# Optimization experiments

Hardware: AMD Instinct MI355X
Metric: run time of the kernel (lower is better)

Reference implementation:

```python
import jax, jax.numpy as jnp
import numpy as np

E = 1024   # embedding_dim
H = 16     # num_head
D = 64     # dim_head (E == H*D)
R = 8      # LoRA rank
BATCH = 2
SEQ = 2048
EPS = 1e-6


def setup_inputs() -> dict:
    key = jax.random.key(0)
    ks = jax.random.split(key, 16)
    s = 0.02
    return {
        "y": jax.random.normal(ks[0], (BATCH, SEQ, E), jnp.float32),
        "Wqkv": jax.random.normal(ks[1], (3 * E, E), jnp.float32) * s,
        "bqkv": jax.random.normal(ks[2], (3 * E,), jnp.float32) * s,
        "Wmsa": jax.random.normal(ks[3], (E, E), jnp.float32) * s,
        "Bq": jax.random.normal(ks[4], (E, R), jnp.float32) * s,
        "Aq": jax.random.normal(ks[5], (R, E), jnp.float32) * s,
        "Bk": jax.random.normal(ks[6], (E, R), jnp.float32) * s,
        "Ak": jax.random.normal(ks[7], (R, E), jnp.float32) * s,
        "Bv": jax.random.normal(ks[8], (E, R), jnp.float32) * s,
        "Av": jax.random.normal(ks[9], (R, E), jnp.float32) * s,
        "Bo": jax.random.normal(ks[10], (E, R), jnp.float32) * s,
        "Ao": jax.random.normal(ks[11], (R, E), jnp.float32) * s,
        "gamma": jnp.ones((E,), jnp.float32),
        "beta": jnp.zeros((E,), jnp.float32),
        "i": 0,
    }


def reference(y, Wqkv, bqkv, Wmsa, Bq, Aq, Bk, Ak, Bv, Av, Bo, Ao, gamma, beta, i):
    B, S, En = y.shape
    # fused QKV projection: nn.Linear -> y @ W.T + b
    qkv = (y @ Wqkv.T + bqkv).reshape(B, S, 3, H, D).transpose(2, 0, 3, 1, 4)
    Q, K, V = qkv[0], qkv[1], qkv[2]          # each [B,H,S,D]

    def lora_delta(Bw, Aw):
        # torch: y @ (B.weight @ A.weight), reshaped to heads
        return (y @ (Bw @ Aw)).reshape(B, S, H, D).transpose(0, 2, 1, 3)

    Q = Q + lora_delta(Bq, Aq)
    K = K + lora_delta(Bk, Ak)
    V = V + lora_delta(Bv, Av)

    scale = jnp.asarray(np.sqrt(D), y.dtype)
    scores = jnp.einsum('bhqd,bhkd->bhqk', Q, K) / scale
    attn = jax.nn.softmax(scores, axis=-1)
    o = jnp.einsum('bhqk,bhkd->bhqd', attn, V)          # [B,H,S,D]
    o = o.transpose(0, 2, 1, 3).reshape(B, S, H * D)    # [B,S,E]

    msa = o @ Wmsa.T + o @ (Bo @ Ao)
    res = msa + y

    mu = jnp.mean(res, axis=-1, keepdims=True)
    var = jnp.var(res, axis=-1, keepdims=True)
    return (res - mu) * jax.lax.rsqrt(var + EPS) * gamma + beta
```

## Files before the change

kernel.cpp:

```cpp
#include <hip/hip_runtime.h>
#include <hip/hip_bf16.h>
#include <stdint.h>

typedef __attribute__((ext_vector_type(8))) short short8;
typedef __attribute__((ext_vector_type(4))) float f32x4;

typedef const __attribute__((address_space(1))) void gv_t;
typedef __attribute__((address_space(3))) void lv_t;

#define SCQ 0.18033688011112042f

__device__ __forceinline__ void gl_lds16(const void* g, void* l) {
    __builtin_amdgcn_global_load_lds((gv_t*)g, (lv_t*)l, 16, 0, 0);
}

__device__ __forceinline__ unsigned short f2bf(float f) {
    union { float f; unsigned int u; } v; v.f = f;
    unsigned int r = v.u + 0x7fffu + ((v.u >> 16) & 1u);
    return (unsigned short)(r >> 16);
}

__device__ __forceinline__ float bf2f(unsigned short u) {
    union { unsigned int i; float f; } v; v.i = ((unsigned int)u) << 16; return v.f;
}

__device__ __forceinline__ unsigned int pack2bf(float a, float b) {
    union { __hip_bfloat162 h2; unsigned int u; } cv;
    cv.h2 = __float22bfloat162_rn(make_float2(a, b));
    return cv.u;
}

__device__ __forceinline__ f32x4 zero4() { f32x4 z = {0.f, 0.f, 0.f, 0.f}; return z; }

__global__ void k_prep(const float* __restrict__ y,
                       const float* __restrict__ Wqkv, const float* __restrict__ Wmsa,
                       const float* __restrict__ Bq, const float* __restrict__ Aq,
                       const float* __restrict__ Bk, const float* __restrict__ Ak,
                       const float* __restrict__ Bv, const float* __restrict__ Av,
                       const float* __restrict__ Bo, const float* __restrict__ Ao,
                       unsigned short* __restrict__ wout, unsigned short* __restrict__ yb) {
    const int bid = blockIdx.x;
    if (bid < 16384) {
        int idx = bid * 256 + threadIdx.x;
        int n = idx >> 10, k = idx & 1023;
        int sel = n >> 10, n0 = n & 1023;
        const float* Bp = (sel == 0) ? Bq : (sel == 1) ? Bk : (sel == 2) ? Bv : Bo;
        const float* Ap = (sel == 0) ? Aq : (sel == 1) ? Ak : (sel == 2) ? Av : Ao;
        float acc = (sel < 3) ? Wqkv[idx] : Wmsa[idx - 3145728];
        float4 b0 = *(const float4*)(Bp + k * 8);
        float4 b1 = *(const float4*)(Bp + k * 8 + 4);
        acc += b0.x * Ap[0 * 1024 + n0] + b0.y * Ap[1 * 1024 + n0]
             + b0.z * Ap[2 * 1024 + n0] + b0.w * Ap[3 * 1024 + n0]
             + b1.x * Ap[4 * 1024 + n0] + b1.y * Ap[5 * 1024 + n0]
             + b1.z * Ap[6 * 1024 + n0] + b1.w * Ap[7 * 1024 + n0];
        wout[idx] = f2bf(acc * ((sel == 0) ? SCQ : 1.0f));
    } else {
        int i = ((bid - 16384) * 256 + threadIdx.x) * 4;
        float4 v = *(const float4*)(y + i);
        union { unsigned short u[4]; uint2 w; } o;
        o.u[0] = f2bf(v.x); o.u[1] = f2bf(v.y); o.u[2] = f2bf(v.z); o.u[3] = f2bf(v.w);
        *(uint2*)(yb + i) = o.w;
    }
}

template <int TM, int EPI, int MINW, int XMAP>
__global__ __launch_bounds__(256, MINW) void k_gemm(const unsigned short* __restrict__ Ag,
                                                    const unsigned short* __restrict__ Bg,
                                                    const float* __restrict__ bias,
                                                    const float* __restrict__ yres,
                                                    unsigned short* __restrict__ vtg,
                                                    void* __restrict__ Cout,
                                                    int M, int N, int K, int Kst) {
    constexpr int WAVES_N = 256 / TM;
    constexpr int WN = TM / 2;
    constexpr int NI = WN / 16;
    constexpr int ACALLS = TM / 64;
    constexpr int ASZ = 2 * TM * 32;
    __shared__ unsigned short SH[ASZ + 2 * 128 * 32];
    unsigned short* As0 = SH;
    unsigned short* Bs0 = SH + ASZ;
    const int flat = threadIdx.x;
    int m0, n0, koff = 0, split = 0;
    if constexpr (XMAP == 1) {
        int id = blockIdx.x, xcd = id & 7, j = id >> 3;
        int yy = (xcd & 3) * 8 + j / 12;
        int xx = (xcd >> 2) * 12 + j % 12;
        m0 = yy * TM; n0 = xx * 128;
    } else if constexpr (XMAP == 2) {
        int id = blockIdx.x, xcd = id & 7, j = id >> 3;
        split = xcd >> 2;
        int yy = (xcd & 3) * 8 + (j >> 3);
        int xx = j & 7;
        m0 = yy * TM; n0 = xx * 128; koff = split * 512;
    } else {
        m0 = blockIdx.y * TM; n0 = blockIdx.x * 128;
    }
    const int lane = flat & 63, wave = flat >> 6;
    const int l16 = lane & 15, quad = lane >> 4;
    const int wm = (wave / WAVES_N) * 64, wn = (wave % WAVES_N) * WN;

    f32x4 acc[4][NI];
    #pragma unroll
    for (int mi = 0; mi < 4; ++mi)
        #pragma unroll
        for (int ni = 0; ni < NI; ++ni) acc[mi][ni] = zero4();

    const unsigned short* ap = Ag + (size_t)(m0 + (flat >> 2)) * Kst + koff + (flat & 3) * 8;
    const unsigned short* bp = Bg + (size_t)(n0 + (flat >> 2)) * Kst + koff + (flat & 3) * 8;
    const size_t rstep = (size_t)64 * Kst;

    #pragma unroll
    for (int c = 0; c < ACALLS; ++c) gl_lds16(ap + c * rstep, &As0[c * 2048 + flat * 8]);
    gl_lds16(bp,         &Bs0[flat * 8]);
    gl_lds16(bp + rstep, &Bs0[2048 + flat * 8]);
    ap += 32; bp += 32;
    __syncthreads();

    for (int k0 = 0; k0 < K; k0 += 32) {
        const int cur = (k0 >> 5) & 1;
        if (k0 + 32 < K) {
            const int nxt = cur ^ 1;
            #pragma unroll
            for (int c = 0; c < ACALLS; ++c) gl_lds16(ap + c * rstep, &As0[nxt * TM * 32 + c * 2048 + flat * 8]);
            gl_lds16(bp,         &Bs0[nxt * 4096 + flat * 8]);
            gl_lds16(bp + rstep, &Bs0[nxt * 4096 + 2048 + flat * 8]);
            ap += 32; bp += 32;
        }

        short8 af[4], bfr[NI];
        #pragma unroll
        for (int i = 0; i < 4; ++i) af[i] = *(const short8*)&As0[cur * TM * 32 + (wm + i * 16 + l16) * 32 + quad * 8];
        #pragma unroll
        for (int i = 0; i < NI; ++i) bfr[i] = *(const short8*)&Bs0[cur * 4096 + (wn + i * 16 + l16) * 32 + quad * 8];
        #pragma unroll
        for (int mi = 0; mi < 4; ++mi)
            #pragma unroll
            for (int ni = 0; ni < NI; ++ni)
                acc[mi][ni] = __builtin_amdgcn_mfma_f32_16x16x32_bf16(af[mi], bfr[ni], acc[mi][ni], 0, 0, 0);

        __syncthreads();
    }

    if constexpr (EPI == 0) {
        unsigned short* C = (unsigned short*)Cout;
        if (n0 < 2048) {
            #pragma unroll
            for (int ni = 0; ni < NI; ++ni) {
                int col = n0 + wn + ni * 16 + l16;
                float bv = bias[col] * ((col < 1024) ? SCQ : 1.0f);
                #pragma unroll
                for (int mi = 0; mi < 4; ++mi) {
                    int row = m0 + wm + mi * 16 + quad * 4;
                    #pragma unroll
                    for (int r = 0; r < 4; ++r)
                        C[(size_t)(row + r) * N + col] = f2bf(acc[mi][ni][r] + bv);
                }
            }
        } else {
            if constexpr (TM == 128) {
                #pragma unroll
                for (int ni = 0; ni < NI; ++ni) {
                    int c = wn + ni * 16 + l16;
                    float bv = bias[n0 + c];
                    int sw = (c & 7) << 3;
                    #pragma unroll
                    for (int mi = 0; mi < 4; ++mi) {
                        int row = wm + mi * 16 + quad * 4;
                        uint2 w;
                        w.x = pack2bf(acc[mi][ni][0] + bv, acc[mi][ni][1] + bv);
                        w.y = pack2bf(acc[mi][ni][2] + bv, acc[mi][ni][3] + bv);
                        *(uint2*)&SH[c * 128 + (row ^ sw)] = w;
                    }
                }
                __syncthreads();
                const int bb = m0 >> 11, ss = m0 & 2047;
                #pragma unroll
                for (int p = 0; p < 4; ++p) {
                    int c = p * 32 + (flat >> 3);
                    int col = n0 + c;
                    int hh = (col - 2048) >> 6, dd = col & 63;
                    unsigned short* dst = vtg + (size_t)(hh * 64 + dd) * 2048
                                              + (size_t)bb * 2097152 + ss;
                    int sw = (c & 7) << 3;
                    #pragma unroll
                    for (int hf = 0; hf < 2; ++hf) {
                        int off = hf * 64 + (flat & 7) * 8;
                        uint4 v = *(const uint4*)&SH[c * 128 + (off ^ sw)];
                        *(uint4*)(dst + off) = v;
                    }
                }
            }
        }
    } else if constexpr (EPI == 1) {
        float* C = (float*)Cout;
        #pragma unroll
        for (int ni = 0; ni < NI; ++ni) {
            int col = n0 + wn + ni * 16 + l16;
            #pragma unroll
            for (int mi = 0; mi < 4; ++mi) {
                int row = m0 + wm + mi * 16 + quad * 4;
                #pragma unroll
                for (int r = 0; r < 4; ++r)
                    C[(size_t)(row + r) * N + col] = acc[mi][ni][r] + yres[(size_t)(row + r) * N + col];
            }
        }
    } else {
        unsigned short* C = (unsigned short*)Cout + (size_t)split * 4194304;
        #pragma unroll
        for (int ni = 0; ni < NI; ++ni) {
            int col = n0 + wn + ni * 16 + l16;
            #pragma unroll
            for (int mi = 0; mi < 4; ++mi) {
                int row = m0 + wm + mi * 16 + quad * 4;
                #pragma unroll
                for (int r = 0; r < 4; ++r)
                    C[(size_t)(row + r) * N + col] = f2bf(acc[mi][ni][r]);
            }
        }
    }
}

__global__ __launch_bounds__(256, 2) void k_attn(const unsigned short* __restrict__ qkv,
                                                 const unsigned short* __restrict__ vtg,
                                                 unsigned short* __restrict__ o) {
    __shared__ unsigned short LDS[16384];
    unsigned short* Qs = LDS;
    unsigned short* Ks0 = LDS;
    unsigned short* Vt0 = LDS + 8192;

    const int t = threadIdx.x;
    const int lane = t & 63, wave = t >> 6;
    const int l16 = lane & 15, quad = lane >> 4;
    const int l8 = l16 & 7;
    const int id = blockIdx.x;
    const int xcd = id & 7, loc = id >> 3;
    const int qb = loc & 15;
    const int P = xcd + 8 * (loc >> 4);
    const int h = P & 15, b = P >> 4;
    const int q0 = qb * 128;

    const unsigned short* qbase = qkv + (size_t)(b * 2048) * 3072 + h * 64;
    const unsigned short* kbase = qbase + 1024;
    const unsigned short* vtbase = vtg + (size_t)((b * 16 + h) * 64) * 2048;

    #pragma unroll
    for (int i = 0; i < 4; ++i) {
        int B = i * 256 + t;
        int row = B >> 3, c = (B & 7) ^ (row & 7);
        gl_lds16(qbase + (size_t)(q0 + row) * 3072 + c * 8, &Qs[B * 8]);
    }

    const int B0 = t, B1 = t + 256;
    const int r0 = B0 >> 3, c0 = (B0 & 7) ^ (r0 & 7);
    const int r1 = B1 >> 3, c1 = (B1 & 7) ^ (r1 & 7);
    const unsigned short* kp0 = kbase + (size_t)r0 * 3072 + c0 * 8;
    const unsigned short* kp1 = kbase + (size_t)r1 * 3072 + c1 * 8;
    const unsigned short* vp0 = vtbase + (size_t)r0 * 2048 + c0 * 8;
    const unsigned short* vp1 = vtbase + (size_t)r1 * 2048 + c1 * 8;

    __syncthreads();

    short8 qf[2][2];
    #pragma unroll
    for (int ni = 0; ni < 2; ++ni)
        #pragma unroll
        for (int kk = 0; kk < 2; ++kk)
            qf[ni][kk] = *(const short8*)&Qs[(wave * 32 + ni * 16 + l16) * 64 + ((kk * 4 + quad) ^ l8) * 8];

    __syncthreads();

    gl_lds16(kp0, &Ks0[B0 * 8]);
    gl_lds16(kp1, &Ks0[B1 * 8]);
    gl_lds16(vp0, &Vt0[B0 * 8]);
    gl_lds16(vp1, &Vt0[B1 * 8]);
    kp0 += 64 * 3072; kp1 += 64 * 3072; vp0 += 64; vp1 += 64;

    f32x4 acc_o[2][4];
    #pragma unroll
    for (int mo = 0; mo < 2; ++mo)
        #pragma unroll
        for (int nd = 0; nd < 4; ++nd) acc_o[mo][nd] = zero4();
    f32x4 acc_l[2] = {zero4(), zero4()};
    const f32x4 Z4 = zero4();
    short8 ones;
    #pragma unroll
    for (int i = 0; i < 8; ++i) ones[i] = (short)0x3F80;

    __syncthreads();

    for (int j = 0; j < 32; ++j) {
        const unsigned short* Ks = Ks0 + (j & 1) * 4096;
        const unsigned short* Vt = Vt0 + (j & 1) * 4096;

        if (j < 31) {
            unsigned short* Kn = Ks0 + ((j + 1) & 1) * 4096;
            unsigned short* Vn = Vt0 + ((j + 1) & 1) * 4096;
            gl_lds16(kp0, &Kn[B0 * 8]);
            gl_lds16(kp1, &Kn[B1 * 8]);
            gl_lds16(vp0, &Vn[B0 * 8]);
            gl_lds16(vp1, &Vn[B1 * 8]);
            kp0 += 64 * 3072; kp1 += 64 * 3072; vp0 += 64; vp1 += 64;
        }

        f32x4 sacc[4][2];
        #pragma unroll
        for (int mi = 0; mi < 4; ++mi) {
            short8 kf0 = *(const short8*)&Ks[(mi * 16 + l16) * 64 + ((0 + quad) ^ l8) * 8];
            short8 kf1 = *(const short8*)&Ks[(mi * 16 + l16) * 64 + ((4 + quad) ^ l8) * 8];
            #pragma unroll
            for (int ni = 0; ni < 2; ++ni) {
                sacc[mi][ni] = __builtin_amdgcn_mfma_f32_16x16x32_bf16(kf0, qf[ni][0], Z4, 0, 0, 0);
                sacc[mi][ni] = __builtin_amdgcn_mfma_f32_16x16x32_bf16(kf1, qf[ni][1], sacc[mi][ni], 0, 0, 0);
            }
        }

        short8 pf[2][2];
        #pragma unroll
        for (int ni = 0; ni < 2; ++ni)
            #pragma unroll
            for (int kk = 0; kk < 2; ++kk) {
                float e00 = __builtin_amdgcn_exp2f(sacc[2 * kk][ni][0]);
                float e01 = __builtin_amdgcn_exp2f(sacc[2 * kk][ni][1]);
                float e02 = __builtin_amdgcn_exp2f(sacc[2 * kk][ni][2]);
                float e03 = __builtin_amdgcn_exp2f(sacc[2 * kk][ni][3]);
                float e10 = __builtin_amdgcn_exp2f(sacc[2 * kk + 1][ni][0]);
                float e11 = __builtin_amdgcn_exp2f(sacc[2 * kk + 1][ni][1]);
                float e12 = __builtin_amdgcn_exp2f(sacc[2 * kk + 1][ni][2]);
                float e13 = __builtin_amdgcn_exp2f(sacc[2 * kk + 1][ni][3]);
                unsigned int a0 = pack2bf(e00, e01);
                unsigned int b0 = pack2bf(e10, e11);
                unsigned int a1 = pack2bf(e02, e03);
                unsigned int b1 = pack2bf(e12, e13);
                asm volatile("v_permlane32_swap_b32 %0, %1\n\t"
                             "v_permlane16_swap_b32 %0, %1"
                             : "+v"(a0), "+v"(b0));
                asm volatile("v_permlane32_swap_b32 %0, %1\n\t"
                             "v_permlane16_swap_b32 %0, %1"
                             : "+v"(a1), "+v"(b1));
                union { unsigned int u[4]; short8 s; } cv;
                cv.u[0] = a0; cv.u[1] = a1; cv.u[2] = b0; cv.u[3] = b1;
                pf[ni][kk] = cv.s;
            }

        #pragma unroll
        for (int kk = 0; kk < 2; ++kk) {
            #pragma unroll
            for (int mo = 0; mo < 2; ++mo)
                acc_l[mo] = __builtin_amdgcn_mfma_f32_16x16x32_bf16(pf[mo][kk], ones, acc_l[mo], 0, 0, 0);
            #pragma unroll
            for (int nd = 0; nd < 4; ++nd) {
                short8 vf = *(const short8*)&Vt[(nd * 16 + l16) * 64 + ((kk * 4 + quad) ^ l8) * 8];
                #pragma unroll
                for (int mo = 0; mo < 2; ++mo)
                    acc_o[mo][nd] = __builtin_amdgcn_mfma_f32_16x16x32_bf16(pf[mo][kk], vf, acc_o[mo][nd], 0, 0, 0);
            }
        }

        __syncthreads();
    }

    #pragma unroll
    for (int mo = 0; mo < 2; ++mo)
        #pragma unroll
        for (int rr = 0; rr < 4; ++rr) {
            float inv = 1.0f / acc_l[mo][rr];
            int qg = q0 + wave * 32 + mo * 16 + quad * 4 + rr;
            size_t base = ((size_t)(b * 2048 + qg)) * 1024 + h * 64;
            #pragma unroll
            for (int nd = 0; nd < 4; ++nd)
                o[base + nd * 16 + l16] = f2bf(acc_o[mo][nd][rr] * inv);
        }
}

__global__ __launch_bounds__(256) void k_ln(const float* __restrict__ y,
                                            const unsigned short* __restrict__ p0,
                                            const unsigned short* __restrict__ p1,
                                            const float* __restrict__ g,
                                            const float* __restrict__ be,
                                            float* __restrict__ out) {
    const int row = blockIdx.x * 4 + (threadIdx.x >> 6);
    const int lane = threadIdx.x & 63;
    const float* xr = y + (size_t)row * 1024;
    const unsigned short* ar = p0 + (size_t)row * 1024;
    const unsigned short* br = p1 + (size_t)row * 1024;
    float4 v[4];
    float s = 0.f, sq = 0.f;
    #pragma unroll
    for (int i = 0; i < 4; ++i) {
        float4 vy = *(const float4*)(xr + i * 256 + lane * 4);
        union { uint2 w; unsigned short u[4]; } ua, ub;
        ua.w = *(const uint2*)(ar + i * 256 + lane * 4);
        ub.w = *(const uint2*)(br + i * 256 + lane * 4);
        v[i].x = vy.x + bf2f(ua.u[0]) + bf2f(ub.u[0]);
        v[i].y = vy.y + bf2f(ua.u[1]) + bf2f(ub.u[1]);
        v[i].z = vy.z + bf2f(ua.u[2]) + bf2f(ub.u[2]);
        v[i].w = vy.w + bf2f(ua.u[3]) + bf2f(ub.u[3]);
        s  += v[i].x + v[i].y + v[i].z + v[i].w;
        sq += v[i].x * v[i].x + v[i].y * v[i].y + v[i].z * v[i].z + v[i].w * v[i].w;
    }
    #pragma unroll
    for (int off = 32; off; off >>= 1) { s += __shfl_down(s, off); sq += __shfl_down(sq, off); }
    s = __shfl(s, 0); sq = __shfl(sq, 0);
    float mu = s * (1.f / 1024.f);
    float var = sq * (1.f / 1024.f) - mu * mu;
    float rstd = rsqrtf(var + 1e-6f);
    float* orow = out + (size_t)row * 1024;
    #pragma unroll
    for (int i = 0; i < 4; ++i) {
        float4 gg = *(const float4*)(g + i * 256 + lane * 4);
        float4 bb = *(const float4*)(be + i * 256 + lane * 4);
        float4 ov;
        ov.x = (v[i].x - mu) * rstd * gg.x + bb.x;
        ov.y = (v[i].y - mu) * rstd * gg.y + bb.y;
        ov.z = (v[i].z - mu) * rstd * gg.z + bb.z;
        ov.w = (v[i].w - mu) * rstd * gg.w + bb.w;
        *(float4*)(orow + i * 256 + lane * 4) = ov;
    }
}

extern "C" void kernel_launch(void* const* d_in, const int* in_sizes, int n_in,
                              void* d_out, int out_size, void* d_ws, size_t ws_size,
                              hipStream_t stream) {
    (void)in_sizes; (void)n_in; (void)out_size; (void)ws_size;
    const float* y    = (const float*)d_in[0];
    const float* Wqkv = (const float*)d_in[1];
    const float* bqkv = (const float*)d_in[2];
    const float* Wmsa = (const float*)d_in[3];
    const float* Bq = (const float*)d_in[4];
    const float* Aq = (const float*)d_in[5];
    const float* Bk = (const float*)d_in[6];
    const float* Ak = (const float*)d_in[7];
    const float* Bv = (const float*)d_in[8];
    const float* Av = (const float*)d_in[9];
    const float* Bo = (const float*)d_in[10];
    const float* Ao = (const float*)d_in[11];
    const float* gamma = (const float*)d_in[12];
    const float* beta  = (const float*)d_in[13];

    char* ws = (char*)d_ws;
    unsigned short* yb   = (unsigned short*)(ws);
    unsigned short* weq  = (unsigned short*)(ws + (8u  << 20));
    unsigned short* qkv  = (unsigned short*)(ws + (16u << 20));
    unsigned short* vtg  = (unsigned short*)(ws + (40u << 20));
    unsigned short* wem  = weq + 3145728;
    unsigned short* obuf = yb;
    unsigned short* resb = qkv;

    k_prep<<<17408, 256, 0, stream>>>(y, Wqkv, Wmsa, Bq, Aq, Bk, Ak, Bv, Av, Bo, Ao, weq, yb);
    k_gemm<128, 0, 3, 1><<<768, 256, 0, stream>>>(yb, weq, bqkv, nullptr, vtg, (void*)qkv, 4096, 3072, 1024, 1024);
    k_attn<<<512, 256, 0, stream>>>(qkv, vtg, obuf);
    k_gemm<128, 2, 3, 2><<<512, 256, 0, stream>>>(obuf, wem, nullptr, nullptr, nullptr, (void*)resb, 4096, 1024, 512, 1024);
    k_ln  <<<1024, 256, 0, stream>>>(y, resb, resb + 4194304, gamma, beta, (float*)d_out);
}
```

Measured before the change: 208.0 us.

## Split attention KV range in two with partial outputs and reduction kernel

The attention kernel now uses 128-thread blocks, each wave handling 64 query rows, and splits the key/value sequence into two halves. This doubles the grid to 1024 blocks. Each block writes unnormalized bf16 partial outputs and row sums, and a new reduction kernel adds the two partials and normalizes them. The intent is more parallelism and more Q reuse per K/V tile, at the cost of an extra launch, extra memory traffic, and bf16 rounding of the partial sums. The unused fp32 residual epilogue of the GEMM is also removed.

Measured after the change: 214.0 us. 1.03x slower.

```diff
diff --git a/kernel.cpp b/kernel.cpp
--- a/kernel.cpp
+++ b/kernel.cpp
@@ -191,19 +191,6 @@
                 }
             }
         }
-    } else if constexpr (EPI == 1) {
-        float* C = (float*)Cout;
-        #pragma unroll
-        for (int ni = 0; ni < NI; ++ni) {
-            int col = n0 + wn + ni * 16 + l16;
-            #pragma unroll
-            for (int mi = 0; mi < 4; ++mi) {
-                int row = m0 + wm + mi * 16 + quad * 4;
-                #pragma unroll
-                for (int r = 0; r < 4; ++r)
-                    C[(size_t)(row + r) * N + col] = acc[mi][ni][r] + yres[(size_t)(row + r) * N + col];
-            }
-        }
     } else {
         unsigned short* C = (unsigned short*)Cout + (size_t)split * 4194304;
         #pragma unroll
@@ -220,9 +207,10 @@
     }
 }
 
-__global__ __launch_bounds__(256, 2) void k_attn(const unsigned short* __restrict__ qkv,
+__global__ __launch_bounds__(128, 2) void k_attn(const unsigned short* __restrict__ qkv,
                                                  const unsigned short* __restrict__ vtg,
-                                                 unsigned short* __restrict__ o) {
+                                                 unsigned short* __restrict__ opart,
+                                                 float* __restrict__ lout) {
     __shared__ unsigned short LDS[16384];
     unsigned short* Qs = LDS;
     unsigned short* Ks0 = LDS;
@@ -236,51 +224,55 @@
     const int xcd = id & 7, loc = id >> 3;
     const int qb = loc & 15;
     const int P = xcd + 8 * (loc >> 4);
-    const int h = P & 15, b = P >> 4;
+    const int h = P & 15, rest = P >> 4;
+    const int b = rest & 1, split = rest >> 1;
     const int q0 = qb * 128;
 
     const unsigned short* qbase = qkv + (size_t)(b * 2048) * 3072 + h * 64;
-    const unsigned short* kbase = qbase + 1024;
-    const unsigned short* vtbase = vtg + (size_t)((b * 16 + h) * 64) * 2048;
-
-    #pragma unroll
-    for (int i = 0; i < 4; ++i) {
-        int B = i * 256 + t;
+    const unsigned short* kbase = qbase + 1024 + (size_t)(split * 1024) * 3072;
+    const unsigned short* vtbase = vtg + (size_t)((b * 16 + h) * 64) * 2048 + split * 1024;
+
+    #pragma unroll
+    for (int i = 0; i < 8; ++i) {
+        int B = i * 128 + t;
         int row = B >> 3, c = (B & 7) ^ (row & 7);
         gl_lds16(qbase + (size_t)(q0 + row) * 3072 + c * 8, &Qs[B * 8]);
     }
 
-    const int B0 = t, B1 = t + 256;
-    const int r0 = B0 >> 3, c0 = (B0 & 7) ^ (r0 & 7);
-    const int r1 = B1 >> 3, c1 = (B1 & 7) ^ (r1 & 7);
-    const unsigned short* kp0 = kbase + (size_t)r0 * 3072 + c0 * 8;
-    const unsigned short* kp1 = kbase + (size_t)r1 * 3072 + c1 * 8;
-    const unsigned short* vp0 = vtbase + (size_t)r0 * 2048 + c0 * 8;
-    const unsigned short* vp1 = vtbase + (size_t)r1 * 2048 + c1 * 8;
+    const unsigned short* kp[4];
+    const unsigned short* vp[4];
+    #pragma unroll
+    for (int i = 0; i < 4; ++i) {
+        int B = i * 128 + t;
+        int r = B >> 3, c = (B & 7) ^ (r & 7);
+        kp[i] = kbase + (size_t)r * 3072 + c * 8;
+        vp[i] = vtbase + (size_t)r * 2048 + c * 8;
+    }
 
     __syncthreads();
 
-    short8 qf[2][2];
-    #pragma unroll
-    for (int ni = 0; ni < 2; ++ni)
+    short8 qf[4][2];
+    #pragma unroll
+    for (int ni = 0; ni < 4; ++ni)
         #pragma unroll
         for (int kk = 0; kk < 2; ++kk)
-            qf[ni][kk] = *(const short8*)&Qs[(wave * 32 + ni * 16 + l16) * 64 + ((kk * 4 + quad) ^ l8) * 8];
+            qf[ni][kk] = *(const short8*)&Qs[(wave * 64 + ni * 16 + l16) * 64 + ((kk * 4 + quad) ^ l8) * 8];
 
     __syncthreads();
 
-    gl_lds16(kp0, &Ks0[B0 * 8]);
-    gl_lds16(kp1, &Ks0[B1 * 8]);
-    gl_lds16(vp0, &Vt0[B0 * 8]);
-    gl_lds16(vp1, &Vt0[B1 * 8]);
-    kp0 += 64 * 3072; kp1 += 64 * 3072; vp0 += 64; vp1 += 64;
-
-    f32x4 acc_o[2][4];
-    #pragma unroll
-    for (int mo = 0; mo < 2; ++mo)
+    #pragma unroll
+    for (int i = 0; i < 4; ++i) {
+        gl_lds16(kp[i], &Ks0[(i * 128 + t) * 8]);
+        gl_lds16(vp[i], &Vt0[(i * 128 + t) * 8]);
+        kp[i] += 64 * 3072; vp[i] += 64;
+    }
+
+    f32x4 acc_o[4][4];
+    #pragma unroll
+    for (int mo = 0; mo < 4; ++mo)
         #pragma unroll
         for (int nd = 0; nd < 4; ++nd) acc_o[mo][nd] = zero4();
-    f32x4 acc_l[2] = {zero4(), zero4()};
+    f32x4 acc_l[4] = {zero4(), zero4(), zero4(), zero4()};
     const f32x4 Z4 = zero4();
     short8 ones;
     #pragma unroll
@@ -288,35 +280,36 @@
 
     __syncthreads();
 
-    for (int j = 0; j < 32; ++j) {
+    for (int j = 0; j < 16; ++j) {
         const unsigned short* Ks = Ks0 + (j & 1) * 4096;
         const unsigned short* Vt = Vt0 + (j & 1) * 4096;
 
-        if (j < 31) {
+        if (j < 15) {
             unsigned short* Kn = Ks0 + ((j + 1) & 1) * 4096;
             unsigned short* Vn = Vt0 + ((j + 1) & 1) * 4096;
-            gl_lds16(kp0, &Kn[B0 * 8]);
-            gl_lds16(kp1, &Kn[B1 * 8]);
-            gl_lds16(vp0, &Vn[B0 * 8]);
-            gl_lds16(vp1, &Vn[B1 * 8]);
-            kp0 += 64 * 3072; kp1 += 64 * 3072; vp0 += 64; vp1 += 64;
-        }
-
-        f32x4 sacc[4][2];
+            #pragma unroll
+            for (int i = 0; i < 4; ++i) {
+                gl_lds16(kp[i], &Kn[(i * 128 + t) * 8]);
+                gl_lds16(vp[i], &Vn[(i * 128 + t) * 8]);
+                kp[i] += 64 * 3072; vp[i] += 64;
+            }
+        }
+
+        f32x4 sacc[4][4];
         #pragma unroll
         for (int mi = 0; mi < 4; ++mi) {
             short8 kf0 = *(const short8*)&Ks[(mi * 16 + l16) * 64 + ((0 + quad) ^ l8) * 8];
             short8 kf1 = *(const short8*)&Ks[(mi * 16 + l16) * 64 + ((4 + quad) ^ l8) * 8];
             #pragma unroll
-            for (int ni = 0; ni < 2; ++ni) {
+            for (int ni = 0; ni < 4; ++ni) {
                 sacc[mi][ni] = __builtin_amdgcn_mfma_f32_16x16x32_bf16(kf0, qf[ni][0], Z4, 0, 0, 0);
                 sacc[mi][ni] = __builtin_amdgcn_mfma_f32_16x16x32_bf16(kf1, qf[ni][1], sacc[mi][ni], 0, 0, 0);
             }
         }
 
-        short8 pf[2][2];
-        #pragma unroll
-        for (int ni = 0; ni < 2; ++ni)
+        short8 pf[4][2];
+        #pragma unroll
+        for (int ni = 0; ni < 4; ++ni)
             #pragma unroll
             for (int kk = 0; kk < 2; ++kk) {
                 float e00 = __builtin_amdgcn_exp2f(sacc[2 * kk][ni][0]);
@@ -345,13 +338,13 @@
         #pragma unroll
         for (int kk = 0; kk < 2; ++kk) {
             #pragma unroll
-            for (int mo = 0; mo < 2; ++mo)
+            for (int mo = 0; mo < 4; ++mo)
                 acc_l[mo] = __builtin_amdgcn_mfma_f32_16x16x32_bf16(pf[mo][kk], ones, acc_l[mo], 0, 0, 0);
             #pragma unroll
             for (int nd = 0; nd < 4; ++nd) {
                 short8 vf = *(const short8*)&Vt[(nd * 16 + l16) * 64 + ((kk * 4 + quad) ^ l8) * 8];
                 #pragma unroll
-                for (int mo = 0; mo < 2; ++mo)
+                for (int mo = 0; mo < 4; ++mo)
                     acc_o[mo][nd] = __builtin_amdgcn_mfma_f32_16x16x32_bf16(pf[mo][kk], vf, acc_o[mo][nd], 0, 0, 0);
             }
         }
@@ -359,17 +352,43 @@
         __syncthreads();
     }
 
-    #pragma unroll
-    for (int mo = 0; mo < 2; ++mo)
+    const size_t obase = ((size_t)(split * 32 + b * 16 + h)) * 2048;
+    #pragma unroll
+    for (int mo = 0; mo < 4; ++mo)
         #pragma unroll
         for (int rr = 0; rr < 4; ++rr) {
-            float inv = 1.0f / acc_l[mo][rr];
-            int qg = q0 + wave * 32 + mo * 16 + quad * 4 + rr;
-            size_t base = ((size_t)(b * 2048 + qg)) * 1024 + h * 64;
+            int qg = q0 + wave * 64 + mo * 16 + quad * 4 + rr;
+            unsigned short* op = opart + (obase + qg) * 64;
             #pragma unroll
             for (int nd = 0; nd < 4; ++nd)
-                o[base + nd * 16 + l16] = f2bf(acc_o[mo][nd][rr] * inv);
-        }
+                op[nd * 16 + l16] = f2bf(acc_o[mo][nd][rr]);
+            if (l16 == 0)
+                lout[(size_t)(b * 2048 + qg) * 1536 + 1024 + split * 16 + h] = acc_l[mo][rr];
+        }
+}
+
+__global__ __launch_bounds__(256) void k_ored(const unsigned short* __restrict__ opart,
+                                              const float* __restrict__ lin,
+                                              unsigned short* __restrict__ o) {
+    const int bid = blockIdx.x;
+    const int bh = bid >> 7, chunk = bid & 127;
+    const int t = threadIdx.x;
+    const int qloc = t >> 4, dd = (t & 15) * 4;
+    const int q = chunk * 16 + qloc;
+    const int b = bh >> 4, h = bh & 15;
+    const size_t i0 = ((size_t)bh * 2048 + q) * 64 + dd;
+    const size_t i1 = ((size_t)(32 + bh) * 2048 + q) * 64 + dd;
+    uint2 p0 = *(const uint2*)(opart + i0);
+    uint2 p1 = *(const uint2*)(opart + i1);
+    const size_t lrow = (size_t)(b * 2048 + q) * 1536 + 1024;
+    float inv = 1.0f / (lin[lrow + h] + lin[lrow + 16 + h]);
+    union { uint2 w; unsigned short u[4]; } a, c;
+    a.w = p0;
+    union { uint2 w; unsigned short u[4]; } bb; bb.w = p1;
+    #pragma unroll
+    for (int i = 0; i < 4; ++i)
+        c.u[i] = f2bf((bf2f(a.u[i]) + bf2f(bb.u[i])) * inv);
+    *(uint2*)(o + ((size_t)(b * 2048 + q)) * 1024 + h * 64 + dd) = c.w;
 }
 
 __global__ __launch_bounds__(256) void k_ln(const float* __restrict__ y,
@@ -442,13 +461,15 @@
     unsigned short* weq  = (unsigned short*)(ws + (8u  << 20));
     unsigned short* qkv  = (unsigned short*)(ws + (16u << 20));
     unsigned short* vtg  = (unsigned short*)(ws + (40u << 20));
+    unsigned short* opart= (unsigned short*)(ws + (48u << 20));
     unsigned short* wem  = weq + 3145728;
     unsigned short* obuf = yb;
     unsigned short* resb = qkv;
 
     k_prep<<<17408, 256, 0, stream>>>(y, Wqkv, Wmsa, Bq, Aq, Bk, Ak, Bv, Av, Bo, Ao, weq, yb);
     k_gemm<128, 0, 3, 1><<<768, 256, 0, stream>>>(yb, weq, bqkv, nullptr, vtg, (void*)qkv, 4096, 3072, 1024, 1024);
-    k_attn<<<512, 256, 0, stream>>>(qkv, vtg, obuf);
+    k_attn<<<1024, 128, 0, stream>>>(qkv, vtg, opart, (float*)qkv);
+    k_ored<<<4096, 256, 0, stream>>>(opart, (const float*)qkv, obuf);
     k_gemm<128, 2, 3, 2><<<512, 256, 0, stream>>>(obuf, wem, nullptr, nullptr, nullptr, (void*)resb, 4096, 1024, 512, 1024);
     k_ln  <<<1024, 256, 0, stream>>>(y, resb, resb + 4194304, gamma, beta, (float*)d_out);
 }
```
